# Optimization experiments

Measured on AMD Instinct MI355X. Metric: run time of the kernel, lower is better.

## Reference

```python
import jax, jax.numpy as jnp
import numpy as np

B, C, H, W = 8, 256, 128, 128
M = C // 8  # query/key reduced channels (scale=8)
EPS = 1e-6


def setup_inputs() -> dict:
    key = jax.random.key(0)
    ks = jax.random.split(key, 9)
    s = 0.02
    return {
        "x": jax.random.normal(ks[0], (B, C, H, W), jnp.float32),
        "wq": jax.random.normal(ks[1], (M, C), jnp.float32) * s,
        "bq": jax.random.normal(ks[2], (M,), jnp.float32) * s,
        "wk": jax.random.normal(ks[3], (M, C), jnp.float32) * s,
        "bk": jax.random.normal(ks[4], (M,), jnp.float32) * s,
        "wv": jax.random.normal(ks[5], (C, C), jnp.float32) * s,
        "bv": jax.random.normal(ks[6], (C,), jnp.float32) * s,
        "gamma_k": jax.random.normal(ks[7], (1,), jnp.float32) * 0.1,
        "gamma_c": jax.random.normal(ks[8], (1,), jnp.float32) * 0.1,
    }


def _conv1x1(x, w, b):
    # 1x1 conv == per-pixel linear map over channels
    return jnp.einsum("oc,bchw->bohw", w, x) + b[None, :, None, None]


def reference(x, wq, bq, wk, bk, wv, bv, gamma_k, gamma_c):
    b, c, h, w = x.shape
    n = h * w

    # ---- KernelAttentionModule (softplus linear attention, O(n)) ----
    Q = jax.nn.softplus(_conv1x1(x, wq, bq)).reshape(b, -1, n).transpose(0, 2, 1)  # [b,n,m]
    K = jax.nn.softplus(_conv1x1(x, wk, bk)).reshape(b, -1, n)                      # [b,m,n]
    V = _conv1x1(x, wv, bv).reshape(b, c, n)                                        # [b,c,n]
    KV = jnp.einsum("bmn,bcn->bmc", K, V)                                           # [b,m,c]
    norm = 1.0 / jnp.einsum("bnm,bm->bn", Q, jnp.sum(K, axis=-1) + EPS)             # [b,n]
    weight_value = jnp.einsum("bnm,bmc,bn->bcn", Q, KV, norm).reshape(b, c, h, w)
    kam = x + gamma_k * weight_value

    # ---- ChannelAttentionModule (channel bmm attention) ----
    pq = x.reshape(b, c, n)
    energy = jnp.einsum("bcn,bdn->bcd", pq, pq)                                     # [b,c,c]
    energy_new = jnp.max(energy, axis=-1, keepdims=True) - energy
    attn = jax.nn.softmax(energy_new, axis=-1)
    cam = gamma_c * jnp.einsum("bcd,bdn->bcn", attn, pq).reshape(b, c, h, w)

    return kam + cam
```

## Files before the change

### kernel.cpp

```cpp
#include <hip/hip_runtime.h>
#include <math.h>

#define NPIX 16384
#define CH 256
#define MDIM 32
#define NB 8
#define EPSF 1e-6f
#define SPLIT 16
#define KCH (NPIX / SPLIT)

#define XKPART_F32OFF 16777216ull

typedef short short4v __attribute__((ext_vector_type(4)));
typedef short short8 __attribute__((ext_vector_type(8)));
typedef _Float16 half8 __attribute__((ext_vector_type(8)));
typedef float f32x4 __attribute__((ext_vector_type(4)));

__device__ inline unsigned short f2bf(float v) {
    unsigned u = __builtin_bit_cast(unsigned, v);
    unsigned r = u + 0x7FFFu + ((u >> 16) & 1u);
    return (unsigned short)(r >> 16);
}
__device__ inline float bf2f(unsigned short h) {
    unsigned u = (unsigned)h << 16;
    return __builtin_bit_cast(float, u);
}

__global__ void k_prep(const float* __restrict__ wq, const float* __restrict__ wk,
                       unsigned short* __restrict__ WQB, unsigned short* __restrict__ WKB)
{
    int i = blockIdx.x * 256 + threadIdx.x;
    WQB[i] = f2bf(wq[i]);
    WKB[i] = f2bf(wk[i]);
}

__global__ __launch_bounds__(256, 4) void k_kx(
    const float* __restrict__ x,
    const unsigned short* __restrict__ WKB, const unsigned short* __restrict__ WQB,
    const float* __restrict__ bk, const float* __restrict__ bq,
    unsigned short* __restrict__ xkpart, float* __restrict__ Ksum,
    unsigned short* __restrict__ Qg)
{
    __shared__ unsigned short xs[CH * 72];
    __shared__ unsigned short ksm[MDIM * 64];
    const int b = blockIdx.y, t = blockIdx.x, n0 = t * 64, tid = threadIdx.x;
    const int w = tid >> 6, l = tid & 63;
    const int li = l & 15, lg = l >> 4;
    const float* xb = x + (size_t)b * CH * NPIX;

    #pragma unroll
    for (int s = 0; s < 8; ++s) {
        int e8 = tid + s * 256;
        int c = e8 >> 3, j8 = e8 & 7;
        const float* src = xb + (size_t)c * NPIX + n0 + j8 * 8;
        float4 v0 = *(const float4*)src;
        float4 v1 = *(const float4*)(src + 4);
        float vv[8] = {v0.x, v0.y, v0.z, v0.w, v1.x, v1.y, v1.z, v1.w};
        short8 p;
        #pragma unroll
        for (int e = 0; e < 8; ++e) p[e] = (short)f2bf(vv[e]);
        const int g = j8 ^ (c & 7) ^ ((c >> 3) & 7);
        *(short8*)&xs[c * 72 + g * 8] = p;
    }
    __syncthreads();

    {
        f32x4 accK[2], accQ[2];
        #pragma unroll
        for (int i = 0; i < 2; ++i) {
            accK[i] = (f32x4){0.f, 0.f, 0.f, 0.f};
            accQ[i] = (f32x4){0.f, 0.f, 0.f, 0.f};
        }
        const int n = w * 16 + li;
        const int gn = n >> 3, inn = n & 7;
        #pragma unroll
        for (int kc = 0; kc < 8; ++kc) {
            short8 bxw;
            #pragma unroll
            for (int e = 0; e < 8; ++e) {
                const int d = kc * 32 + lg * 8 + e;
                const int g = gn ^ e ^ ((kc * 4 + lg) & 7);
                bxw[e] = (short)xs[d * 72 + g * 8 + inn];
            }
            #pragma unroll
            for (int i = 0; i < 2; ++i) {
                const size_t wo = (size_t)(i * 16 + li) * CH + kc * 32 + lg * 8;
                short8 kw = *(const short8*)(WKB + wo);
                short8 qw = *(const short8*)(WQB + wo);
                accK[i] = __builtin_amdgcn_mfma_f32_16x16x32_bf16(kw, bxw, accK[i], 0, 0, 0);
                accQ[i] = __builtin_amdgcn_mfma_f32_16x16x32_bf16(qw, bxw, accQ[i], 0, 0, 0);
            }
        }
        unsigned short* qp = Qg + ((size_t)b * NPIX + n0 + n) * MDIM;
        #pragma unroll
        for (int i = 0; i < 2; ++i) {
            short4v q4;
            #pragma unroll
            for (int q = 0; q < 4; ++q) {
                const int m = i * 16 + lg * 4 + q;
                float kv = accK[i][q] + bk[m];
                kv = fmaxf(kv, 0.f) + log1pf(expf(-fabsf(kv)));
                ksm[m * 64 + (n ^ ((m & 7) << 3))] = f2bf(kv);
                float qv = accQ[i][q] + bq[m];
                qv = fmaxf(qv, 0.f) + log1pf(expf(-fabsf(qv)));
                q4[q] = (short)f2bf(qv);
            }
            *(short4v*)(qp + i * 16 + lg * 4) = q4;
        }
    }
    __syncthreads();

    if (tid < MDIM) {
        float s = 0.f;
        #pragma unroll
        for (int j = 0; j < 64; ++j)
            s += bf2f(ksm[tid * 64 + (j ^ ((tid & 7) << 3))]);
        atomicAdd(&Ksum[b * MDIM + tid], s);
    }

    f32x4 axk[4][2];
    #pragma unroll
    for (int i = 0; i < 4; ++i)
        #pragma unroll
        for (int j = 0; j < 2; ++j) axk[i][j] = (f32x4){0.f, 0.f, 0.f, 0.f};

    #pragma unroll
    for (int ks2 = 0; ks2 < 2; ++ks2) {
        const int nc = ks2 * 32 + lg * 8;
        short8 kfr[2];
        #pragma unroll
        for (int j = 0; j < 2; ++j) {
            const int m = j * 16 + li;
            kfr[j] = *(const short8*)&ksm[m * 64 + (nc ^ ((m & 7) << 3))];
        }
        #pragma unroll
        for (int i = 0; i < 4; ++i) {
            const int d = w * 64 + i * 16 + li;
            const int g = (nc >> 3) ^ (d & 7) ^ ((d >> 3) & 7);
            short8 xf = *(const short8*)&xs[d * 72 + g * 8];
            #pragma unroll
            for (int j = 0; j < 2; ++j)
                axk[i][j] = __builtin_amdgcn_mfma_f32_16x16x32_bf16(xf, kfr[j], axk[i][j], 0, 0, 0);
        }
    }

    unsigned short* xkp = xkpart + (size_t)(b * 256 + t) * MDIM * CH;
    #pragma unroll
    for (int i = 0; i < 4; ++i)
        #pragma unroll
        for (int j = 0; j < 2; ++j) {
            short4v pk;
            #pragma unroll
            for (int q = 0; q < 4; ++q) pk[q] = (short)f2bf(axk[i][j][q]);
            *(short4v*)(xkp + (size_t)(j * 16 + li) * CH + w * 64 + i * 16 + lg * 4) = pk;
        }
}

__global__ void k_xkreduce(const unsigned short* __restrict__ xkpart,
                           float* __restrict__ XKR) {
    const int b = blockIdx.x >> 5, m = blockIdx.x & 31, d = threadIdx.x;
    const int t0 = blockIdx.y * 64;
    float s = 0.f;
    #pragma unroll 4
    for (int t = t0; t < t0 + 64; ++t)
        s += bf2f(xkpart[(((size_t)b * 256 + t) * MDIM + m) * CH + d]);
    atomicAdd(&XKR[((size_t)b * MDIM + m) * CH + d], s);
}

__global__ void k_kv(const float* __restrict__ wv, const float* __restrict__ bv,
                     const float* __restrict__ XKR, const float* __restrict__ Ksum,
                     unsigned short* __restrict__ KVTb) {
    const int b = blockIdx.x, q = blockIdx.y;
    const int ci = threadIdx.x & 63, mg = threadIdx.x >> 6;
    const int c = q * 64 + ci;
    float s[8];
    const float bvc = bv[c];
    #pragma unroll
    for (int i = 0; i < 8; ++i) s[i] = bvc * Ksum[b * MDIM + mg * 8 + i];
    #pragma unroll 4
    for (int d = 0; d < CH; ++d) {
        float w = wv[(size_t)c * CH + d];
        #pragma unroll
        for (int i = 0; i < 8; ++i)
            s[i] = fmaf(w, XKR[((size_t)b * MDIM + mg * 8 + i) * CH + d], s[i]);
    }
    short8 p;
    #pragma unroll
    for (int i = 0; i < 8; ++i) p[i] = (short)f2bf(s[i]);
    *(short8*)(KVTb + ((size_t)b * CH + c) * MDIM + mg * 8) = p;
}

__global__ __launch_bounds__(256, 4) void k_gram(const float* __restrict__ x,
                                                 float* __restrict__ enpart)
{
    __shared__ unsigned short As[128 * 72];
    __shared__ unsigned short Bs[128 * 72];

    const int tid = threadIdx.x;
    const int rt = (blockIdx.x == 2) ? 1 : 0;
    const int ct = (blockIdx.x == 0) ? 0 : 1;
    const bool diag = (rt == ct);
    const int sp = blockIdx.y, b = blockIdx.z;
    const int r0 = rt * 128, c0 = ct * 128;
    const float* xb = x + (size_t)b * CH * NPIX;
    const int k0base = sp * KCH;

    unsigned short* Bs_p = diag ? As : Bs;

    const int wave = tid >> 6, lane = tid & 63;
    const int wr = wave >> 1, wc = wave & 1;

    f32x4 acc[4][4];
    #pragma unroll
    for (int i = 0; i < 4; ++i)
        #pragma unroll
        for (int j = 0; j < 4; ++j)
            acc[i][j] = (f32x4){0.f, 0.f, 0.f, 0.f};

    const int oct = tid & 7;
    const int frow = tid >> 3;

    for (int kk = 0; kk < KCH; kk += 64) {
        __syncthreads();
        const int k0 = k0base + kk;
        #pragma unroll
        for (int half = 0; half < 2; ++half) {
            if (half && diag) continue;
            const int rowbase = half ? c0 : r0;
            unsigned short* Hs = half ? Bs : As;
            #pragma unroll
            for (int s = 0; s < 4; ++s) {
                const int r = frow + s * 32;
                const float* src = xb + (size_t)(rowbase + r) * NPIX + k0 + oct * 8;
                float4 v0 = *(const float4*)src;
                float4 v1 = *(const float4*)(src + 4);
                float vv[8] = {v0.x, v0.y, v0.z, v0.w, v1.x, v1.y, v1.z, v1.w};
                short8 p;
                #pragma unroll
                for (int e = 0; e < 8; ++e)
                    p[e] = __builtin_bit_cast(short, (_Float16)vv[e]);
                *(short8*)&Hs[r * 72 + oct * 8] = p;
            }
        }
        __syncthreads();

        #pragma unroll
        for (int ks2 = 0; ks2 < 2; ++ks2) {
            short8 a4[4], b4[4];
            const int rbase = wr * 64 + (lane & 15);
            const int cbase = wc * 64 + (lane & 15);
            const int koff = ks2 * 32 + (lane >> 4) * 8;
            #pragma unroll
            for (int f = 0; f < 4; ++f) {
                a4[f] = *(const short8*)&As[(rbase + f * 16) * 72 + koff];
                b4[f] = *(const short8*)&Bs_p[(cbase + f * 16) * 72 + koff];
            }
            #pragma unroll
            for (int i = 0; i < 4; ++i)
                #pragma unroll
                for (int j = 0; j < 4; ++j)
                    acc[i][j] = __builtin_amdgcn_mfma_f32_16x16x32_f16(
                        __builtin_bit_cast(half8, a4[i]),
                        __builtin_bit_cast(half8, b4[j]), acc[i][j], 0, 0, 0);
        }
    }

    float* ep = enpart + (size_t)(sp * NB + b) * (CH * CH);
    const int rw = (lane >> 4) * 4;
    const int cw = lane & 15;
    #pragma unroll
    for (int i = 0; i < 4; ++i)
        #pragma unroll
        for (int j = 0; j < 4; ++j) {
            const int row = r0 + wr * 64 + i * 16 + rw;
            const int col = c0 + wc * 64 + j * 16 + cw;
            #pragma unroll
            for (int q = 0; q < 4; ++q) {
                float v = acc[i][j][q];
                ep[(size_t)(row + q) * CH + col] = v;
                if (!diag) ep[(size_t)col * CH + (row + q)] = v;
            }
        }
}

__global__ void k_softmax(const float* __restrict__ enpart,
                          const float* __restrict__ gc,
                          unsigned short* __restrict__ attnb) {
    const int b = blockIdx.x >> 8, c = blockIdx.x & 255;
    const int d = threadIdx.x;
    __shared__ float red[8];
    float e = 0.f;
    #pragma unroll
    for (int sp = 0; sp < SPLIT; ++sp)
        e += enpart[(size_t)(sp * NB + b) * (CH * CH) + (size_t)c * CH + d];
    float mn = e;
    #pragma unroll
    for (int o = 1; o < 64; o <<= 1) mn = fminf(mn, __shfl_xor(mn, o));
    if ((d & 63) == 0) red[d >> 6] = mn;
    __syncthreads();
    mn = fminf(fminf(red[0], red[1]), fminf(red[2], red[3]));
    float w = expf(mn - e);
    float s = w;
    #pragma unroll
    for (int o = 1; o < 64; o <<= 1) s += __shfl_xor(s, o);
    if ((d & 63) == 0) red[4 + (d >> 6)] = s;
    __syncthreads();
    s = red[4] + red[5] + red[6] + red[7];
    attnb[((size_t)(b * CH) + c) * CH + d] = f2bf(gc[0] * w / s);
}

__global__ __launch_bounds__(256, 4) void k_final(
    const float* __restrict__ x, const unsigned short* __restrict__ Qg,
    const unsigned short* __restrict__ KVTb, const float* __restrict__ Ksum,
    const unsigned short* __restrict__ attnb, const float* __restrict__ gk,
    float* __restrict__ out)
{
    __shared__ uint2 xsTv[4096];
    unsigned char* xsT = (unsigned char*)xsTv;
    const int b = blockIdx.y, n0 = blockIdx.x * 64, tid = threadIdx.x;
    const int w = tid >> 6, l = tid & 63;
    const int li = l & 15, lg = l >> 4;
    const float* xb = x + (size_t)b * CH * NPIX;

    short8 qb[4];
    #pragma unroll
    for (int j = 0; j < 4; ++j)
        qb[j] = *(const short8*)(Qg +
            ((size_t)b * NPIX + n0 + j * 16 + li) * MDIM + lg * 8);
    float4 ks0 = *(const float4*)(Ksum + b * MDIM + lg * 8);
    float4 ks1 = *(const float4*)(Ksum + b * MDIM + lg * 8 + 4);
    const float kse[8] = {ks0.x + EPSF, ks0.y + EPSF, ks0.z + EPSF, ks0.w + EPSF,
                          ks1.x + EPSF, ks1.y + EPSF, ks1.z + EPSF, ks1.w + EPSF};

    {
        const int n4 = li * 4;
        const bool o1 = lg & 1, o2 = (lg >> 1) & 1;
        #pragma unroll 4
        for (int p = 0; p < 16; ++p) {
            const int d0 = w * 64 + p * 4;
            float4 vv = *(const float4*)(xb + (size_t)(d0 + lg) * NPIX + n0 + n4);
            float v0 = vv.x, v1 = vv.y, v2 = vv.z, v3 = vv.w;
            float r1 = __shfl_xor(o1 ? v0 : v1, 16);
            float r2 = __shfl_xor(o1 ? v2 : v3, 16);
            float a0 = o1 ? r1 : v0, a1 = o1 ? v1 : r1;
            float a2 = o1 ? r2 : v2, a3 = o1 ? v3 : r2;
            float r3 = __shfl_xor(o2 ? a0 : a2, 32);
            float r4 = __shfl_xor(o2 ? a1 : a3, 32);
            float b0 = o2 ? r3 : a0, b1 = o2 ? r4 : a1;
            float b2 = o2 ? a2 : r3, b3 = o2 ? a3 : r4;
            const int nl = n4 + lg;
            unsigned lo = (unsigned)f2bf(b0) | ((unsigned)f2bf(b1) << 16);
            unsigned hi = (unsigned)f2bf(b2) | ((unsigned)f2bf(b3) << 16);
            const int off = nl * 512 +
                ((2 * d0) ^ ((nl & 7) << 4) ^ (((nl >> 3) & 1) << 3));
            *(uint2*)(xsT + off) = make_uint2(lo, hi);
        }
    }

    f32x4 acc[4][4];
    #pragma unroll
    for (int i = 0; i < 4; ++i)
        #pragma unroll
        for (int j = 0; j < 4; ++j)
            acc[i][j] = (f32x4){0.f, 0.f, 0.f, 0.f};

    {
        const float gkv = gk[0];
        short8 qs[4];
        #pragma unroll
        for (int j = 0; j < 4; ++j) {
            float qf[8];
            float den = 0.f;
            #pragma unroll
            for (int e = 0; e < 8; ++e) {
                qf[e] = bf2f((unsigned short)qb[j][e]);
                den = fmaf(qf[e], kse[e], den);
            }
            den += __shfl_xor(den, 16);
            den += __shfl_xor(den, 32);
            const float nrm = gkv / den;
            #pragma unroll
            for (int e = 0; e < 8; ++e) qs[j][e] = (short)f2bf(qf[e] * nrm);
        }
        #pragma unroll
        for (int i = 0; i < 4; ++i) {
            short8 ka = *(const short8*)(KVTb +
                ((size_t)b * CH + w * 64 + i * 16 + li) * MDIM + lg * 8);
            #pragma unroll
            for (int j = 0; j < 4; ++j)
                acc[i][j] = __builtin_amdgcn_mfma_f32_16x16x32_bf16(qs[j], ka, acc[i][j], 0, 0, 0);
        }
    }
    __syncthreads();

    const unsigned short* ab = attnb + (size_t)b * CH * CH;
    for (int kk = 0; kk < CH; kk += 32) {
        short8 bx[4];
        #pragma unroll
        for (int j = 0; j < 4; ++j) {
            const int nf = j * 16 + li;
            const int d2 = 2 * (kk + lg * 8);
            const int sw = ((nf & 7) << 4) ^ (((nf >> 3) & 1) << 3);
            uint2 h0 = *(const uint2*)(xsT + nf * 512 + (d2 ^ sw));
            uint2 h1 = *(const uint2*)(xsT + nf * 512 + ((d2 + 8) ^ sw));
            int4 tmp = make_int4(h0.x, h0.y, h1.x, h1.y);
            bx[j] = __builtin_bit_cast(short8, tmp);
        }
        #pragma unroll
        for (int i = 0; i < 4; ++i) {
            short8 af = *(const short8*)(ab +
                (size_t)(w * 64 + i * 16 + li) * CH + kk + lg * 8);
            #pragma unroll
            for (int j = 0; j < 4; ++j)
                acc[i][j] = __builtin_amdgcn_mfma_f32_16x16x32_bf16(bx[j], af, acc[i][j], 0, 0, 0);
        }
    }

    float* outb = out + (size_t)b * CH * NPIX;
    #pragma unroll
    for (int i = 0; i < 4; ++i) {
        const int c = w * 64 + i * 16 + li;
        #pragma unroll
        for (int j = 0; j < 4; ++j) {
            const size_t idx = (size_t)c * NPIX + n0 + j * 16 + lg * 4;
            float4 xv = *(const float4*)(xb + idx);
            float4 v = make_float4(xv.x + acc[i][j][0], xv.y + acc[i][j][1],
                                   xv.z + acc[i][j][2], xv.w + acc[i][j][3]);
            *(float4*)(outb + idx) = v;
        }
    }
}

extern "C" void kernel_launch(void* const* d_in, const int* in_sizes, int n_in,
                              void* d_out, int out_size, void* d_ws, size_t ws_size,
                              hipStream_t stream)
{
    const float* x  = (const float*)d_in[0];
    const float* wq = (const float*)d_in[1];
    const float* bq = (const float*)d_in[2];
    const float* wk = (const float*)d_in[3];
    const float* bk = (const float*)d_in[4];
    const float* wv = (const float*)d_in[5];
    const float* bv = (const float*)d_in[6];
    const float* gk = (const float*)d_in[7];
    const float* gc = (const float*)d_in[8];
    float* out = (float*)d_out;
    char* wsb = (char*)d_ws;

    unsigned short* ATTB = (unsigned short*)(wsb);
    unsigned short* KVTB = (unsigned short*)(wsb + 1048576);
    float* KSUM = (float*)(wsb + 1179648);
    float* XKR  = (float*)(wsb + 1180672);
    unsigned short* WQB = (unsigned short*)(wsb + 1442816);
    unsigned short* WKB = (unsigned short*)(wsb + 1459200);
    unsigned short* QG  = (unsigned short*)(wsb + 1508352);

    unsigned short* xkpart = (unsigned short*)out;
    float* enpart = out + XKPART_F32OFF;

    hipMemsetAsync(KSUM, 0, 1024 + 262144, stream);

    k_prep<<<dim3(32), dim3(256), 0, stream>>>(wq, wk, WQB, WKB);
    k_kx<<<dim3(NPIX / 64, NB), dim3(256), 0, stream>>>(x, WKB, WQB, bk, bq,
                                                        xkpart, KSUM, QG);
    k_gram<<<dim3(3, SPLIT, NB), dim3(256), 0, stream>>>(x, enpart);
    k_xkreduce<<<dim3(NB * MDIM, 4), dim3(CH), 0, stream>>>(xkpart, XKR);
    k_kv<<<dim3(NB, 4), dim3(256), 0, stream>>>(wv, bv, XKR, KSUM, KVTB);
    k_softmax<<<dim3(NB * CH), dim3(CH), 0, stream>>>(enpart, gc, ATTB);
    k_final<<<dim3(NPIX / 64, NB), dim3(256), 0, stream>>>(x, QG, KVTB, KSUM,
                                                           ATTB, gk, out);
}
```

Measured before the change: 261.6 us.

## Switch bf16 MFMA paths to fp16 and stream gram operands directly from global

```diff
diff --git a/kernel.cpp b/kernel.cpp
--- a/kernel.cpp
+++ b/kernel.cpp
@@ -16,22 +16,19 @@
 typedef _Float16 half8 __attribute__((ext_vector_type(8)));
 typedef float f32x4 __attribute__((ext_vector_type(4)));
 
-__device__ inline unsigned short f2bf(float v) {
-    unsigned u = __builtin_bit_cast(unsigned, v);
-    unsigned r = u + 0x7FFFu + ((u >> 16) & 1u);
-    return (unsigned short)(r >> 16);
-}
-__device__ inline float bf2f(unsigned short h) {
-    unsigned u = (unsigned)h << 16;
-    return __builtin_bit_cast(float, u);
+__device__ inline unsigned short f2h(float v) {
+    return __builtin_bit_cast(unsigned short, (_Float16)v);
+}
+__device__ inline float h2f(unsigned short h) {
+    return (float)__builtin_bit_cast(_Float16, h);
 }
 
 __global__ void k_prep(const float* __restrict__ wq, const float* __restrict__ wk,
                        unsigned short* __restrict__ WQB, unsigned short* __restrict__ WKB)
 {
     int i = blockIdx.x * 256 + threadIdx.x;
-    WQB[i] = f2bf(wq[i]);
-    WKB[i] = f2bf(wk[i]);
+    WQB[i] = f2h(wq[i]);
+    WKB[i] = f2h(wk[i]);
 }
 
 __global__ __launch_bounds__(256, 4) void k_kx(
@@ -58,7 +55,7 @@
         float vv[8] = {v0.x, v0.y, v0.z, v0.w, v1.x, v1.y, v1.z, v1.w};
         short8 p;
         #pragma unroll
-        for (int e = 0; e < 8; ++e) p[e] = (short)f2bf(vv[e]);
+        for (int e = 0; e < 8; ++e) p[e] = (short)f2h(vv[e]);
         const int g = j8 ^ (c & 7) ^ ((c >> 3) & 7);
         *(short8*)&xs[c * 72 + g * 8] = p;
     }
@@ -82,13 +79,14 @@
                 const int g = gn ^ e ^ ((kc * 4 + lg) & 7);
                 bxw[e] = (short)xs[d * 72 + g * 8 + inn];
             }
+            half8 bx = __builtin_bit_cast(half8, bxw);
             #pragma unroll
             for (int i = 0; i < 2; ++i) {
                 const size_t wo = (size_t)(i * 16 + li) * CH + kc * 32 + lg * 8;
-                short8 kw = *(const short8*)(WKB + wo);
-                short8 qw = *(const short8*)(WQB + wo);
-                accK[i] = __builtin_amdgcn_mfma_f32_16x16x32_bf16(kw, bxw, accK[i], 0, 0, 0);
-                accQ[i] = __builtin_amdgcn_mfma_f32_16x16x32_bf16(qw, bxw, accQ[i], 0, 0, 0);
+                half8 kw = __builtin_bit_cast(half8, *(const short8*)(WKB + wo));
+                half8 qw = __builtin_bit_cast(half8, *(const short8*)(WQB + wo));
+                accK[i] = __builtin_amdgcn_mfma_f32_16x16x32_f16(kw, bx, accK[i], 0, 0, 0);
+                accQ[i] = __builtin_amdgcn_mfma_f32_16x16x32_f16(qw, bx, accQ[i], 0, 0, 0);
             }
         }
         unsigned short* qp = Qg + ((size_t)b * NPIX + n0 + n) * MDIM;
@@ -100,10 +98,10 @@
                 const int m = i * 16 + lg * 4 + q;
                 float kv = accK[i][q] + bk[m];
                 kv = fmaxf(kv, 0.f) + log1pf(expf(-fabsf(kv)));
-                ksm[m * 64 + (n ^ ((m & 7) << 3))] = f2bf(kv);
+                ksm[m * 64 + (n ^ ((m & 7) << 3))] = f2h(kv);
                 float qv = accQ[i][q] + bq[m];
                 qv = fmaxf(qv, 0.f) + log1pf(expf(-fabsf(qv)));
-                q4[q] = (short)f2bf(qv);
+                q4[q] = (short)f2h(qv);
             }
             *(short4v*)(qp + i * 16 + lg * 4) = q4;
         }
@@ -114,7 +112,7 @@
         float s = 0.f;
         #pragma unroll
         for (int j = 0; j < 64; ++j)
-            s += bf2f(ksm[tid * 64 + (j ^ ((tid & 7) << 3))]);
+            s += h2f(ksm[tid * 64 + (j ^ ((tid & 7) << 3))]);
         atomicAdd(&Ksum[b * MDIM + tid], s);
     }
 
@@ -127,20 +125,21 @@
     #pragma unroll
     for (int ks2 = 0; ks2 < 2; ++ks2) {
         const int nc = ks2 * 32 + lg * 8;
-        short8 kfr[2];
+        half8 kfr[2];
         #pragma unroll
         for (int j = 0; j < 2; ++j) {
             const int m = j * 16 + li;
-            kfr[j] = *(const short8*)&ksm[m * 64 + (nc ^ ((m & 7) << 3))];
+            kfr[j] = __builtin_bit_cast(half8,
+                *(const short8*)&ksm[m * 64 + (nc ^ ((m & 7) << 3))]);
         }
         #pragma unroll
         for (int i = 0; i < 4; ++i) {
             const int d = w * 64 + i * 16 + li;
             const int g = (nc >> 3) ^ (d & 7) ^ ((d >> 3) & 7);
-            short8 xf = *(const short8*)&xs[d * 72 + g * 8];
+            half8 xf = __builtin_bit_cast(half8, *(const short8*)&xs[d * 72 + g * 8]);
             #pragma unroll
             for (int j = 0; j < 2; ++j)
-                axk[i][j] = __builtin_amdgcn_mfma_f32_16x16x32_bf16(xf, kfr[j], axk[i][j], 0, 0, 0);
+                axk[i][j] = __builtin_amdgcn_mfma_f32_16x16x32_f16(xf, kfr[j], axk[i][j], 0, 0, 0);
         }
     }
 
@@ -151,7 +150,7 @@
         for (int j = 0; j < 2; ++j) {
             short4v pk;
             #pragma unroll
-            for (int q = 0; q < 4; ++q) pk[q] = (short)f2bf(axk[i][j][q]);
+            for (int q = 0; q < 4; ++q) pk[q] = (short)f2h(axk[i][j][q]);
             *(short4v*)(xkp + (size_t)(j * 16 + li) * CH + w * 64 + i * 16 + lg * 4) = pk;
         }
 }
@@ -163,7 +162,7 @@
     float s = 0.f;
     #pragma unroll 4
     for (int t = t0; t < t0 + 64; ++t)
-        s += bf2f(xkpart[(((size_t)b * 256 + t) * MDIM + m) * CH + d]);
+        s += h2f(xkpart[(((size_t)b * 256 + t) * MDIM + m) * CH + d]);
     atomicAdd(&XKR[((size_t)b * MDIM + m) * CH + d], s);
 }
 
@@ -186,16 +185,13 @@
     }
     short8 p;
     #pragma unroll
-    for (int i = 0; i < 8; ++i) p[i] = (short)f2bf(s[i]);
+    for (int i = 0; i < 8; ++i) p[i] = (short)f2h(s[i]);
     *(short8*)(KVTb + ((size_t)b * CH + c) * MDIM + mg * 8) = p;
 }
 
 __global__ __launch_bounds__(256, 4) void k_gram(const float* __restrict__ x,
                                                  float* __restrict__ enpart)
 {
-    __shared__ unsigned short As[128 * 72];
-    __shared__ unsigned short Bs[128 * 72];
-
     const int tid = threadIdx.x;
     const int rt = (blockIdx.x == 2) ? 1 : 0;
     const int ct = (blockIdx.x == 0) ? 0 : 1;
@@ -205,10 +201,9 @@
     const float* xb = x + (size_t)b * CH * NPIX;
     const int k0base = sp * KCH;
 
-    unsigned short* Bs_p = diag ? As : Bs;
-
     const int wave = tid >> 6, lane = tid & 63;
     const int wr = wave >> 1, wc = wave & 1;
+    const int li = lane & 15, lg = lane >> 4;
 
     f32x4 acc[4][4];
     #pragma unroll
@@ -217,57 +212,45 @@
         for (int j = 0; j < 4; ++j)
             acc[i][j] = (f32x4){0.f, 0.f, 0.f, 0.f};
 
-    const int oct = tid & 7;
-    const int frow = tid >> 3;
-
-    for (int kk = 0; kk < KCH; kk += 64) {
-        __syncthreads();
-        const int k0 = k0base + kk;
-        #pragma unroll
-        for (int half = 0; half < 2; ++half) {
-            if (half && diag) continue;
-            const int rowbase = half ? c0 : r0;
-            unsigned short* Hs = half ? Bs : As;
-            #pragma unroll
-            for (int s = 0; s < 4; ++s) {
-                const int r = frow + s * 32;
-                const float* src = xb + (size_t)(rowbase + r) * NPIX + k0 + oct * 8;
-                float4 v0 = *(const float4*)src;
-                float4 v1 = *(const float4*)(src + 4);
-                float vv[8] = {v0.x, v0.y, v0.z, v0.w, v1.x, v1.y, v1.z, v1.w};
-                short8 p;
-                #pragma unroll
-                for (int e = 0; e < 8; ++e)
-                    p[e] = __builtin_bit_cast(short, (_Float16)vv[e]);
-                *(short8*)&Hs[r * 72 + oct * 8] = p;
-            }
-        }
-        __syncthreads();
-
-        #pragma unroll
-        for (int ks2 = 0; ks2 < 2; ++ks2) {
-            short8 a4[4], b4[4];
-            const int rbase = wr * 64 + (lane & 15);
-            const int cbase = wc * 64 + (lane & 15);
-            const int koff = ks2 * 32 + (lane >> 4) * 8;
-            #pragma unroll
-            for (int f = 0; f < 4; ++f) {
-                a4[f] = *(const short8*)&As[(rbase + f * 16) * 72 + koff];
-                b4[f] = *(const short8*)&Bs_p[(cbase + f * 16) * 72 + koff];
-            }
-            #pragma unroll
-            for (int i = 0; i < 4; ++i)
-                #pragma unroll
-                for (int j = 0; j < 4; ++j)
-                    acc[i][j] = __builtin_amdgcn_mfma_f32_16x16x32_f16(
-                        __builtin_bit_cast(half8, a4[i]),
-                        __builtin_bit_cast(half8, b4[j]), acc[i][j], 0, 0, 0);
-        }
+    const float* ap[4];
+    const float* bp[4];
+    #pragma unroll
+    for (int f = 0; f < 4; ++f) {
+        ap[f] = xb + (size_t)(r0 + wr * 64 + f * 16 + li) * NPIX + k0base + lg * 8;
+        bp[f] = xb + (size_t)(c0 + wc * 64 + f * 16 + li) * NPIX + k0base + lg * 8;
+    }
+
+    #pragma unroll 2
+    for (int kk = 0; kk < KCH; kk += 32) {
+        half8 a4[4], b4[4];
+        #pragma unroll
+        for (int f = 0; f < 4; ++f) {
+            float4 v0 = *(const float4*)(ap[f] + kk);
+            float4 v1 = *(const float4*)(ap[f] + kk + 4);
+            a4[f][0] = (_Float16)v0.x; a4[f][1] = (_Float16)v0.y;
+            a4[f][2] = (_Float16)v0.z; a4[f][3] = (_Float16)v0.w;
+            a4[f][4] = (_Float16)v1.x; a4[f][5] = (_Float16)v1.y;
+            a4[f][6] = (_Float16)v1.z; a4[f][7] = (_Float16)v1.w;
+        }
+        #pragma unroll
+        for (int f = 0; f < 4; ++f) {
+            float4 v0 = *(const float4*)(bp[f] + kk);
+            float4 v1 = *(const float4*)(bp[f] + kk + 4);
+            b4[f][0] = (_Float16)v0.x; b4[f][1] = (_Float16)v0.y;
+            b4[f][2] = (_Float16)v0.z; b4[f][3] = (_Float16)v0.w;
+            b4[f][4] = (_Float16)v1.x; b4[f][5] = (_Float16)v1.y;
+            b4[f][6] = (_Float16)v1.z; b4[f][7] = (_Float16)v1.w;
+        }
+        #pragma unroll
+        for (int i = 0; i < 4; ++i)
+            #pragma unroll
+            for (int j = 0; j < 4; ++j)
+                acc[i][j] = __builtin_amdgcn_mfma_f32_16x16x32_f16(a4[i], b4[j], acc[i][j], 0, 0, 0);
     }
 
     float* ep = enpart + (size_t)(sp * NB + b) * (CH * CH);
-    const int rw = (lane >> 4) * 4;
-    const int cw = lane & 15;
+    const int rw = lg * 4;
+    const int cw = li;
     #pragma unroll
     for (int i = 0; i < 4; ++i)
         #pragma unroll
@@ -306,7 +289,7 @@
     if ((d & 63) == 0) red[4 + (d >> 6)] = s;
     __syncthreads();
     s = red[4] + red[5] + red[6] + red[7];
-    attnb[((size_t)(b * CH) + c) * CH + d] = f2bf(gc[0] * w / s);
+    attnb[((size_t)(b * CH) + c) * CH + d] = f2h(gc[0] * w / s);
 }
 
 __global__ __launch_bounds__(256, 4) void k_final(
@@ -349,8 +332,8 @@
             float b0 = o2 ? r3 : a0, b1 = o2 ? r4 : a1;
             float b2 = o2 ? a2 : r3, b3 = o2 ? a3 : r4;
             const int nl = n4 + lg;
-            unsigned lo = (unsigned)f2bf(b0) | ((unsigned)f2bf(b1) << 16);
-            unsigned hi = (unsigned)f2bf(b2) | ((unsigned)f2bf(b3) << 16);
+            unsigned lo = (unsigned)f2h(b0) | ((unsigned)f2h(b1) << 16);
+            unsigned hi = (unsigned)f2h(b2) | ((unsigned)f2h(b3) << 16);
             const int off = nl * 512 +
                 ((2 * d0) ^ ((nl & 7) << 4) ^ (((nl >> 3) & 1) << 3));
             *(uint2*)(xsT + off) = make_uint2(lo, hi);
@@ -366,36 +349,36 @@
 
     {
         const float gkv = gk[0];
-        short8 qs[4];
+        half8 qs[4];
         #pragma unroll
         for (int j = 0; j < 4; ++j) {
             float qf[8];
             float den = 0.f;
             #pragma unroll
             for (int e = 0; e < 8; ++e) {
-                qf[e] = bf2f((unsigned short)qb[j][e]);
+                qf[e] = h2f((unsigned short)qb[j][e]);
                 den = fmaf(qf[e], kse[e], den);
             }
             den += __shfl_xor(den, 16);
             den += __shfl_xor(den, 32);
             const float nrm = gkv / den;
             #pragma unroll
-            for (int e = 0; e < 8; ++e) qs[j][e] = (short)f2bf(qf[e] * nrm);
+            for (int e = 0; e < 8; ++e) qs[j][e] = (_Float16)(qf[e] * nrm);
         }
         #pragma unroll
         for (int i = 0; i < 4; ++i) {
-            short8 ka = *(const short8*)(KVTb +
-                ((size_t)b * CH + w * 64 + i * 16 + li) * MDIM + lg * 8);
+            half8 ka = __builtin_bit_cast(half8, *(const short8*)(KVTb +
+                ((size_t)b * CH + w * 64 + i * 16 + li) * MDIM + lg * 8));
             #pragma unroll
             for (int j = 0; j < 4; ++j)
-                acc[i][j] = __builtin_amdgcn_mfma_f32_16x16x32_bf16(qs[j], ka, acc[i][j], 0, 0, 0);
+                acc[i][j] = __builtin_amdgcn_mfma_f32_16x16x32_f16(qs[j], ka, acc[i][j], 0, 0, 0);
         }
     }
     __syncthreads();
 
     const unsigned short* ab = attnb + (size_t)b * CH * CH;
     for (int kk = 0; kk < CH; kk += 32) {
-        short8 bx[4];
+        half8 bx[4];
         #pragma unroll
         for (int j = 0; j < 4; ++j) {
             const int nf = j * 16 + li;
@@ -404,15 +387,15 @@
             uint2 h0 = *(const uint2*)(xsT + nf * 512 + (d2 ^ sw));
             uint2 h1 = *(const uint2*)(xsT + nf * 512 + ((d2 + 8) ^ sw));
             int4 tmp = make_int4(h0.x, h0.y, h1.x, h1.y);
-            bx[j] = __builtin_bit_cast(short8, tmp);
+            bx[j] = __builtin_bit_cast(half8, tmp);
         }
         #pragma unroll
         for (int i = 0; i < 4; ++i) {
-            short8 af = *(const short8*)(ab +
-                (size_t)(w * 64 + i * 16 + li) * CH + kk + lg * 8);
+            half8 af = __builtin_bit_cast(half8, *(const short8*)(ab +
+                (size_t)(w * 64 + i * 16 + li) * CH + kk + lg * 8));
             #pragma unroll
             for (int j = 0; j < 4; ++j)
-                acc[i][j] = __builtin_amdgcn_mfma_f32_16x16x32_bf16(bx[j], af, acc[i][j], 0, 0, 0);
+                acc[i][j] = __builtin_amdgcn_mfma_f32_16x16x32_f16(bx[j], af, acc[i][j], 0, 0, 0);
         }
     }
 
```

Result: slower. 336.7 us (+28.7%).
